# Kernel optimization log

Hardware: AMD Instinct MI355X
Metric: run time of the kernel (lower is better)

Reference implementation:

```python
import jax, jax.numpy as jnp
import numpy as np

# fp4 e2m1 positive value grid and midpoints between adjacent grid values
_GRID = jnp.array([0.0, 0.5, 1.0, 1.5, 2.0, 3.0, 4.0, 6.0], dtype=jnp.float32)
_MIDS = jnp.array([0.25, 0.75, 1.25, 1.75, 2.5, 3.5, 5.0], dtype=jnp.float32)
BLOCK = 32               # MX block size
E8M0_BIAS = 127
F32_MIN_NORMAL = float(2.0 ** -126)
F4_E2M1_MAX_POW2 = 2     # log2 of largest power-of-two <= 6.0 -> 4.0


def _quantize_fp4(a):
    """Round-to-nearest-even onto the signed e2m1 grid."""
    mag = jnp.clip(jnp.abs(a), 0.0, 6.0)
    idx = jnp.searchsorted(_MIDS, mag, side='left')  # ties round down
    mids_pad = jnp.concatenate([_MIDS, jnp.array([-1.0], jnp.float32)])
    tie = mag == mids_pad[idx]
    idx = jnp.where(tie & (idx % 2 == 1), idx + 1, idx)  # ties-to-even mantissa
    return _GRID[idx] * jnp.where(a < 0, -1.0, 1.0)


def _floor_log2(m):
    """Exact floor(log2(m)) for m > 0, with corrections for fp rounding of log2."""
    e = jnp.floor(jnp.log2(m))
    e = jnp.where(jnp.exp2(e) > m, e - 1.0, e)
    e = jnp.where(jnp.exp2(e + 1.0) <= m, e + 1.0, e)
    return e


def _qdq_mxfp4(x):
    """Quantize-dequantize x to MX fp4_e2m1, block 32, FLOOR scale mode (to_mx + to_dtype)."""
    shp = x.shape
    xb = x.reshape(-1, BLOCK)
    max_abs = jnp.max(jnp.abs(xb), axis=1)
    eps = F32_MIN_NORMAL * (max_abs == 0).astype(jnp.float32)
    pow2 = _floor_log2(max_abs + eps)
    e_unb = jnp.clip(pow2 - F4_E2M1_MAX_POW2, -float(E8M0_BIAS), float(E8M0_BIAS) + 1.0)
    scale = jnp.maximum(jnp.exp2(e_unb), F32_MIN_NORMAL)  # [nblk]
    q = _quantize_fp4(xb / scale[:, None])
    return (q * scale[:, None]).reshape(shp)


def _dequant_weight(weight_packed, weight_scale, out_f, in_f):
    """Unpack uint8-packed fp4 (low nibble first), apply e8m0 block scales."""
    p = weight_packed.astype(jnp.int32)
    low = p & 0xF
    high = (p >> 4) & 0xF
    nib = jnp.stack([low, high], axis=-1).reshape(out_f, in_f)  # interleave low,high
    vals = _GRID[nib & 7] * jnp.where((nib & 8) > 0, -1.0, 1.0)
    s = jnp.exp2(weight_scale.astype(jnp.float32) - E8M0_BIAS)  # get_fp_scale(e8m0)
    return (vals.reshape(-1, BLOCK) * s[:, None]).reshape(out_f, in_f)


def setup_inputs() -> dict:
    key = jax.random.key(0)
    k1, k2, k3 = jax.random.split(key, 3)
    M, IN, OUT = 4096, 4096, 4096
    x = jax.random.normal(k1, (M, IN), dtype=jnp.float32)
    weight_packed = jax.random.randint(k2, (OUT, IN // 2), 0, 256, dtype=jnp.int32)
    weight_scale = jax.random.randint(k3, (OUT * IN // BLOCK,), 0, 135, dtype=jnp.int32)
    return {"x": x, "weight_packed": weight_packed, "weight_scale": weight_scale}


def reference(x, weight_packed, weight_scale):
    out_f = weight_packed.shape[0]
    in_f = weight_packed.shape[1] * 2
    xq = _qdq_mxfp4(x)                                       # qdq_mxfp4(x)
    w_dq = _dequant_weight(weight_packed, weight_scale, out_f, in_f)
    return xq @ w_dq.T                                       # matmul(x, w_dq.t())
```

## Files before the change

### kernel.cpp

```cpp
#include <hip/hip_runtime.h>
#include <stdint.h>

typedef __attribute__((ext_vector_type(4)))  int   intx4;
typedef __attribute__((ext_vector_type(8)))  int   intx8;
typedef __attribute__((ext_vector_type(16))) float floatx16;

#define GLL16(gp, lp)                                                               \
    __builtin_amdgcn_global_load_lds((const __attribute__((address_space(1))) unsigned int*)(gp), \
                                     (__attribute__((address_space(3))) unsigned int*)(lp), 16, 0, 0)
#define GLL4(gp, lp)                                                                \
    __builtin_amdgcn_global_load_lds((const __attribute__((address_space(1))) unsigned int*)(gp), \
                                     (__attribute__((address_space(3))) unsigned int*)(lp), 4, 0, 0)

__device__ __forceinline__ uint32_t enc1(float xv, float inv) {
    float a = fminf(fabsf(xv) * inv, 6.0f);
    int e;
    if (a < 2.0f)      e = (int)rintf(a + a);
    else if (a < 4.0f) e = (int)rintf(a) + 2;
    else               e = (int)rintf(a * 0.5f) + 4;
    return (uint32_t)e | ((__float_as_uint(xv) >> 28) & 8u);
}

__global__ __launch_bounds__(256) void quant_x_kernel(const float* __restrict__ x,
                                                      uint32_t* __restrict__ xq,
                                                      uint8_t* __restrict__ xs) {
    const int gl = blockIdx.x * 256 + threadIdx.x;
    const float4 v = ((const float4*)x)[gl];
    float m = fmaxf(fmaxf(fabsf(v.x), fabsf(v.y)), fmaxf(fabsf(v.z), fabsf(v.w)));
    m = fmaxf(m, __shfl_xor(m, 1));
    m = fmaxf(m, __shfl_xor(m, 2));
    m = fmaxf(m, __shfl_xor(m, 4));
    const unsigned ef = __float_as_uint(m) >> 23;
    const unsigned code = (ef < 3u) ? 1u : (ef - 2u);
    const float inv = __uint_as_float((254u - code) << 23);
    const uint32_t p = enc1(v.x, inv)        | (enc1(v.y, inv) << 4)
                     | (enc1(v.z, inv) << 8) | (enc1(v.w, inv) << 12);
    ((uint16_t*)xq)[gl] = (uint16_t)p;
    if ((gl & 7) == 0) xs[gl >> 3] = (uint8_t)code;
}

__global__ __launch_bounds__(256) void repack_kernel(const int* __restrict__ wp,
                                                     uint32_t* __restrict__ wrep,
                                                     int n4w,
                                                     const int* __restrict__ wsc,
                                                     uint32_t* __restrict__ ws,
                                                     int n4s) {
    const int t = blockIdx.x * 256 + threadIdx.x;
    if (t < n4w) {
        const int4 p = ((const int4*)wp)[t];
        wrep[t] = (uint32_t)(p.x & 0xFF) | ((uint32_t)(p.y & 0xFF) << 8)
                | ((uint32_t)(p.z & 0xFF) << 16) | ((uint32_t)(p.w & 0xFF) << 24);
    } else if (t - n4w < n4s) {
        const int i = t - n4w;
        const int4 p = ((const int4*)wsc)[i];
        ws[i] = (uint32_t)(p.x & 0xFF) | ((uint32_t)(p.y & 0xFF) << 8)
              | ((uint32_t)(p.z & 0xFF) << 16) | ((uint32_t)(p.w & 0xFF) << 24);
    }
}

__global__ __launch_bounds__(256) void tpose_s_kernel(const uint8_t* __restrict__ nat,
                                                      uint8_t* __restrict__ xs_t,
                                                      uint8_t* __restrict__ ws_t,
                                                      int R, int Ck) {
    __shared__ uint8_t raw[128 * 32];
    const int r0 = blockIdx.x * 128;
    const int c0 = blockIdx.y * 32;
    const int t = threadIdx.x;
    {
        const int r = t >> 1, hf = t & 1;
        const uint4 v = *(const uint4*)(nat + (size_t)(r0 + r) * Ck + c0 + hf * 16);
        *(uint4*)(raw + r * 32 + hf * 16) = v;
    }
    __syncthreads();
    const int c = t >> 3, q = t & 7;
    uint32_t d[4];
#pragma unroll
    for (int j = 0; j < 4; ++j) {
        const int mb = q * 16 + j * 4;
        d[j] = (uint32_t)raw[(mb + 0) * 32 + c]
             | ((uint32_t)raw[(mb + 1) * 32 + c] << 8)
             | ((uint32_t)raw[(mb + 2) * 32 + c] << 16)
             | ((uint32_t)raw[(mb + 3) * 32 + c] << 24);
    }
    uint8_t* outp = (r0 < R) ? (xs_t + (size_t)(c0 + c) * R + r0)
                             : (ws_t + (size_t)(c0 + c) * R + (r0 - R));
    *(uint4*)(outp + q * 16) = make_uint4(d[0], d[1], d[2], d[3]);
}

__global__ __launch_bounds__(256) void gemm_mx_kernel(const uint8_t* __restrict__ Apk,
                                                      const uint8_t* __restrict__ Bpk,
                                                      const uint8_t* __restrict__ AsT,
                                                      const uint8_t* __restrict__ BsT,
                                                      float* __restrict__ C,
                                                      int M, int N, int K) {
    __shared__ __align__(16) uint8_t sA[16384];
    __shared__ __align__(16) uint8_t sB[16384];
    __shared__ __align__(16) uint8_t sS[2048];

    const int tid = threadIdx.x;
    const int bm0 = blockIdx.y << 7;
    const int bn0 = blockIdx.x << 7;
    const int wave = tid >> 6;
    const int lane = tid & 63;
    const int wm = (wave >> 1) << 6;
    const int wn = (wave & 1) << 6;
    const int row = lane & 31;
    const int h = lane >> 5;
    const int Kb = K >> 1;

    const uint8_t* Ag[4];
    const uint8_t* Bg[4];
#pragma unroll
    for (int i = 0; i < 4; ++i) {
        const int s = tid + 256 * i;
        const int r = s >> 3;
        const int p = (s & 7) ^ (r & 7);
        Ag[i] = Apk + (size_t)(bm0 + r) * Kb + p * 16;
        Bg[i] = Bpk + (size_t)(bn0 + r) * Kb + p * 16;
    }

    const int st = tid & 127;
    const int sj = st >> 5, si = st & 31;
    const size_t sR = (size_t)((tid < 128) ? M : N);
    const uint8_t* Sg1 = ((tid < 128) ? (AsT + (size_t)sj * M + bm0)
                                      : (BsT + (size_t)sj * N + bn0)) + si * 4;
    const uint8_t* Sg2 = Sg1 + 4 * sR;
    const size_t sAdv = 8 * sR;
    const int soff = ((tid < 128) ? 0 : 1024) + st * 4;

    floatx16 acc[2][2];
#pragma unroll
    for (int a = 0; a < 2; ++a)
#pragma unroll
        for (int b = 0; b < 2; ++b)
#pragma unroll
            for (int r = 0; r < 16; ++r) acc[a][b][r] = 0.f;

    const int nchunk = K >> 8;
    const int ar0 = wm + row, ar1 = wm + 32 + row;
    const int br0 = wn + row, br1 = wn + 32 + row;

    for (int c = 0; c < nchunk; ++c) {
        __syncthreads();
        const size_t koff = (size_t)c << 7;
#pragma unroll
        for (int i = 0; i < 4; ++i) GLL16(Ag[i] + koff, sA + (tid + 256 * i) * 16);
#pragma unroll
        for (int i = 0; i < 4; ++i) GLL16(Bg[i] + koff, sB + (tid + 256 * i) * 16);
        GLL4(Sg1 + (size_t)c * sAdv, sS + soff);
        GLL4(Sg2 + (size_t)c * sAdv, sS + soff + 512);
        __syncthreads();

#pragma unroll
        for (int s = 0; s < 4; ++s) {
            const int kp = 2 * s + h;
            intx4 a4[2], b4[2];
            int sa[2], sb[2];
            a4[0] = *(const intx4*)(sA + ar0 * 128 + ((kp ^ (ar0 & 7)) << 4));
            a4[1] = *(const intx4*)(sA + ar1 * 128 + ((kp ^ (ar1 & 7)) << 4));
            b4[0] = *(const intx4*)(sB + br0 * 128 + ((kp ^ (br0 & 7)) << 4));
            b4[1] = *(const intx4*)(sB + br1 * 128 + ((kp ^ (br1 & 7)) << 4));
            sa[0] = sS[kp * 128 + ar0];
            sa[1] = sS[kp * 128 + ar1];
            sb[0] = sS[1024 + kp * 128 + br0];
            sb[1] = sS[1024 + kp * 128 + br1];
#pragma unroll
            for (int mt = 0; mt < 2; ++mt)
#pragma unroll
                for (int nt = 0; nt < 2; ++nt) {
                    intx8 a8 = {a4[mt][0], a4[mt][1], a4[mt][2], a4[mt][3], 0, 0, 0, 0};
                    intx8 b8 = {b4[nt][0], b4[nt][1], b4[nt][2], b4[nt][3], 0, 0, 0, 0};
                    acc[mt][nt] = __builtin_amdgcn_mfma_scale_f32_32x32x64_f8f6f4(
                        a8, b8, acc[mt][nt], 4, 4, 0, sa[mt], 0, sb[nt]);
                }
        }
    }

#pragma unroll
    for (int mt = 0; mt < 2; ++mt)
#pragma unroll
        for (int nt = 0; nt < 2; ++nt) {
            const int col = bn0 + wn + nt * 32 + row;
#pragma unroll
            for (int g = 0; g < 4; ++g) {
                const int rw = bm0 + wm + mt * 32 + 8 * g + 4 * h;
#pragma unroll
                for (int q = 0; q < 4; ++q)
                    C[(size_t)(rw + q) * N + col] = acc[mt][nt][4 * g + q];
            }
        }
}

extern "C" void kernel_launch(void* const* d_in, const int* in_sizes, int n_in,
                              void* d_out, int out_size, void* d_ws, size_t ws_size,
                              hipStream_t stream) {
    const float* x = (const float*)d_in[0];
    const int* wp = (const int*)d_in[1];
    const int* wsc = (const int*)d_in[2];
    float* out = (float*)d_out;

    const int K = 4096;
    const int M = in_sizes[0] / K;
    const int N = (in_sizes[1] * 2) / K;
    const int kbpr = K / 32;
    const int npack = N * K / 2;

    uint32_t* xq   = (uint32_t*)d_ws;
    uint8_t*  xs   = (uint8_t*)d_ws + (size_t)M * K / 2;
    uint8_t*  ws   = xs + (size_t)M * kbpr;
    uint32_t* wrep = (uint32_t*)(ws + (size_t)N * kbpr);
    uint8_t*  xs_t = (uint8_t*)(wrep + (size_t)npack / 4);
    uint8_t*  ws_t = xs_t + (size_t)M * kbpr;

    const int n4w = npack / 4;
    const int n4s = (N * kbpr) / 4;

    quant_x_kernel<<<(M * K / 4) / 256, 256, 0, stream>>>(x, xq, xs);
    repack_kernel<<<(n4w + n4s + 255) / 256, 256, 0, stream>>>(wp, wrep, n4w,
                                                               wsc, (uint32_t*)ws, n4s);
    dim3 tg(2 * M / 128, kbpr / 32);
    tpose_s_kernel<<<tg, 256, 0, stream>>>(xs, xs_t, ws_t, M, kbpr);

    dim3 grid(N / 128, M / 128);
    gemm_mx_kernel<<<grid, 256, 0, stream>>>((const uint8_t*)xq, (const uint8_t*)wrep,
                                             xs_t, ws_t, out, M, N, K);
}
```

Before: 192.3 us.

## Widen GEMM block tile to 128x256 with 64x128 per-wave tiles

Doubles the N extent of each GEMM workgroup to 256 columns, so each wave computes a 64x128 output tile with 8 MFMA accumulators instead of 4. A-tile loads and A-scale loads are reused across twice as many output columns, which cuts global and LDS traffic per MFMA. Global pointers are also replaced by 32-bit offsets to save registers, and launch bounds ask for 3 workgroups per CU. In exchange, LDS use grows to about 52KB per block, accumulator register pressure doubles, and the grid has half as many workgroups.

```diff
diff --git a/kernel.cpp b/kernel.cpp
--- a/kernel.cpp
+++ b/kernel.cpp
@@ -87,87 +87,91 @@
     *(uint4*)(outp + q * 16) = make_uint4(d[0], d[1], d[2], d[3]);
 }
 
-__global__ __launch_bounds__(256) void gemm_mx_kernel(const uint8_t* __restrict__ Apk,
-                                                      const uint8_t* __restrict__ Bpk,
-                                                      const uint8_t* __restrict__ AsT,
-                                                      const uint8_t* __restrict__ BsT,
-                                                      float* __restrict__ C,
-                                                      int M, int N, int K) {
+__global__ __launch_bounds__(256, 3) void gemm_mx_kernel(const uint8_t* __restrict__ Apk,
+                                                         const uint8_t* __restrict__ Bpk,
+                                                         const uint8_t* __restrict__ AsT,
+                                                         const uint8_t* __restrict__ BsT,
+                                                         float* __restrict__ C,
+                                                         int M, int N, int K) {
     __shared__ __align__(16) uint8_t sA[16384];
-    __shared__ __align__(16) uint8_t sB[16384];
-    __shared__ __align__(16) uint8_t sS[2048];
+    __shared__ __align__(16) uint8_t sB[32768];
+    __shared__ __align__(16) uint8_t sS[3072];
 
     const int tid = threadIdx.x;
     const int bm0 = blockIdx.y << 7;
-    const int bn0 = blockIdx.x << 7;
+    const int bn0 = blockIdx.x << 8;
     const int wave = tid >> 6;
     const int lane = tid & 63;
     const int wm = (wave >> 1) << 6;
-    const int wn = (wave & 1) << 6;
+    const int wn = (wave & 1) << 7;
     const int row = lane & 31;
     const int h = lane >> 5;
     const int Kb = K >> 1;
 
-    const uint8_t* Ag[4];
-    const uint8_t* Bg[4];
+    uint32_t aoff[4], boff[8];
 #pragma unroll
     for (int i = 0; i < 4; ++i) {
         const int s = tid + 256 * i;
         const int r = s >> 3;
         const int p = (s & 7) ^ (r & 7);
-        Ag[i] = Apk + (size_t)(bm0 + r) * Kb + p * 16;
-        Bg[i] = Bpk + (size_t)(bn0 + r) * Kb + p * 16;
-    }
-
-    const int st = tid & 127;
-    const int sj = st >> 5, si = st & 31;
-    const size_t sR = (size_t)((tid < 128) ? M : N);
-    const uint8_t* Sg1 = ((tid < 128) ? (AsT + (size_t)sj * M + bm0)
-                                      : (BsT + (size_t)sj * N + bn0)) + si * 4;
-    const uint8_t* Sg2 = Sg1 + 4 * sR;
-    const size_t sAdv = 8 * sR;
-    const int soff = ((tid < 128) ? 0 : 1024) + st * 4;
-
-    floatx16 acc[2][2];
+        aoff[i] = (uint32_t)((bm0 + r) * Kb + p * 16);
+    }
+#pragma unroll
+    for (int i = 0; i < 8; ++i) {
+        const int s = tid + 256 * i;
+        const int r = s >> 3;
+        const int p = (s & 7) ^ (r & 7);
+        boff[i] = (uint32_t)((bn0 + r) * Kb + p * 16);
+    }
+
+    const uint8_t* SgA  = AsT + (size_t)(tid >> 5) * M + bm0 + (tid & 31) * 4;
+    const uint8_t* SgB1 = BsT + (size_t)(tid >> 6) * N + bn0 + (tid & 63) * 4;
+    const uint8_t* SgB2 = SgB1 + (size_t)4 * N;
+    const size_t sAdvA = (size_t)8 * M;
+    const size_t sAdvB = (size_t)8 * N;
+
+    floatx16 acc[2][4];
 #pragma unroll
     for (int a = 0; a < 2; ++a)
 #pragma unroll
-        for (int b = 0; b < 2; ++b)
+        for (int b = 0; b < 4; ++b)
 #pragma unroll
             for (int r = 0; r < 16; ++r) acc[a][b][r] = 0.f;
 
     const int nchunk = K >> 8;
     const int ar0 = wm + row, ar1 = wm + 32 + row;
-    const int br0 = wn + row, br1 = wn + 32 + row;
 
     for (int c = 0; c < nchunk; ++c) {
         __syncthreads();
-        const size_t koff = (size_t)c << 7;
-#pragma unroll
-        for (int i = 0; i < 4; ++i) GLL16(Ag[i] + koff, sA + (tid + 256 * i) * 16);
-#pragma unroll
-        for (int i = 0; i < 4; ++i) GLL16(Bg[i] + koff, sB + (tid + 256 * i) * 16);
-        GLL4(Sg1 + (size_t)c * sAdv, sS + soff);
-        GLL4(Sg2 + (size_t)c * sAdv, sS + soff + 512);
+        const uint32_t koff = (uint32_t)c << 7;
+#pragma unroll
+        for (int i = 0; i < 4; ++i) GLL16(Apk + aoff[i] + koff, sA + (tid + 256 * i) * 16);
+#pragma unroll
+        for (int i = 0; i < 8; ++i) GLL16(Bpk + boff[i] + koff, sB + (tid + 256 * i) * 16);
+        GLL4(SgA  + (size_t)c * sAdvA, sS + tid * 4);
+        GLL4(SgB1 + (size_t)c * sAdvB, sS + 1024 + tid * 4);
+        GLL4(SgB2 + (size_t)c * sAdvB, sS + 2048 + tid * 4);
         __syncthreads();
 
 #pragma unroll
         for (int s = 0; s < 4; ++s) {
             const int kp = 2 * s + h;
-            intx4 a4[2], b4[2];
-            int sa[2], sb[2];
+            intx4 a4[2], b4[4];
+            int sa[2], sb[4];
             a4[0] = *(const intx4*)(sA + ar0 * 128 + ((kp ^ (ar0 & 7)) << 4));
             a4[1] = *(const intx4*)(sA + ar1 * 128 + ((kp ^ (ar1 & 7)) << 4));
-            b4[0] = *(const intx4*)(sB + br0 * 128 + ((kp ^ (br0 & 7)) << 4));
-            b4[1] = *(const intx4*)(sB + br1 * 128 + ((kp ^ (br1 & 7)) << 4));
             sa[0] = sS[kp * 128 + ar0];
             sa[1] = sS[kp * 128 + ar1];
-            sb[0] = sS[1024 + kp * 128 + br0];
-            sb[1] = sS[1024 + kp * 128 + br1];
+#pragma unroll
+            for (int nt = 0; nt < 4; ++nt) {
+                const int br = wn + nt * 32 + row;
+                b4[nt] = *(const intx4*)(sB + br * 128 + ((kp ^ (br & 7)) << 4));
+                sb[nt] = sS[1024 + kp * 256 + br];
+            }
 #pragma unroll
             for (int mt = 0; mt < 2; ++mt)
 #pragma unroll
-                for (int nt = 0; nt < 2; ++nt) {
+                for (int nt = 0; nt < 4; ++nt) {
                     intx8 a8 = {a4[mt][0], a4[mt][1], a4[mt][2], a4[mt][3], 0, 0, 0, 0};
                     intx8 b8 = {b4[nt][0], b4[nt][1], b4[nt][2], b4[nt][3], 0, 0, 0, 0};
                     acc[mt][nt] = __builtin_amdgcn_mfma_scale_f32_32x32x64_f8f6f4(
@@ -179,7 +183,7 @@
 #pragma unroll
     for (int mt = 0; mt < 2; ++mt)
 #pragma unroll
-        for (int nt = 0; nt < 2; ++nt) {
+        for (int nt = 0; nt < 4; ++nt) {
             const int col = bn0 + wn + nt * 32 + row;
 #pragma unroll
             for (int g = 0; g < 4; ++g) {
@@ -221,7 +225,7 @@
     dim3 tg(2 * M / 128, kbpr / 32);
     tpose_s_kernel<<<tg, 256, 0, stream>>>(xs, xs_t, ws_t, M, kbpr);
 
-    dim3 grid(N / 128, M / 128);
+    dim3 grid(N / 256, M / 128);
     gemm_mx_kernel<<<grid, 256, 0, stream>>>((const uint8_t*)xq, (const uint8_t*)wrep,
                                              xs_t, ws_t, out, M, N, K);
 }
```

Measured after the change: 280.3 us. +45.8%, slower.

## Fuse scale transpose into repack kernel and remap GEMM block order across XCDs

Applied to the files above, without the earlier changes.

Merges the weight-scale packing and the scale-transpose kernels into the repack kernel, so weight scales are read straight from the int32 input and transposed in one pass. This drops one launch and the round trip of the intermediate packed-scale buffer. Separately, the GEMM remaps its linear block id so that consecutive tiles are grouped onto the same XCD (stride nwg/8), aiming for better L2 reuse of A/B tiles. The transpose blocks hardcode 64 row-tiles per column group, which only holds for M=N=4096.

```diff
diff --git a/kernel.cpp b/kernel.cpp
--- a/kernel.cpp
+++ b/kernel.cpp
@@ -41,35 +41,39 @@
 
 __global__ __launch_bounds__(256) void repack_kernel(const int* __restrict__ wp,
                                                      uint32_t* __restrict__ wrep,
-                                                     int n4w,
+                                                     int nwb,
+                                                     const uint8_t* __restrict__ xs,
                                                      const int* __restrict__ wsc,
-                                                     uint32_t* __restrict__ ws,
-                                                     int n4s) {
-    const int t = blockIdx.x * 256 + threadIdx.x;
-    if (t < n4w) {
-        const int4 p = ((const int4*)wp)[t];
-        wrep[t] = (uint32_t)(p.x & 0xFF) | ((uint32_t)(p.y & 0xFF) << 8)
+                                                     uint8_t* __restrict__ xs_t,
+                                                     uint8_t* __restrict__ ws_t,
+                                                     int R, int Ck) {
+    const int bid = blockIdx.x;
+    const int t = threadIdx.x;
+    if (bid < nwb) {
+        const int i = bid * 256 + t;
+        const int4 p = ((const int4*)wp)[i];
+        wrep[i] = (uint32_t)(p.x & 0xFF) | ((uint32_t)(p.y & 0xFF) << 8)
                 | ((uint32_t)(p.z & 0xFF) << 16) | ((uint32_t)(p.w & 0xFF) << 24);
-    } else if (t - n4w < n4s) {
-        const int i = t - n4w;
-        const int4 p = ((const int4*)wsc)[i];
-        ws[i] = (uint32_t)(p.x & 0xFF) | ((uint32_t)(p.y & 0xFF) << 8)
-              | ((uint32_t)(p.z & 0xFF) << 16) | ((uint32_t)(p.w & 0xFF) << 24);
-    }
-}
-
-__global__ __launch_bounds__(256) void tpose_s_kernel(const uint8_t* __restrict__ nat,
-                                                      uint8_t* __restrict__ xs_t,
-                                                      uint8_t* __restrict__ ws_t,
-                                                      int R, int Ck) {
+        return;
+    }
     __shared__ uint8_t raw[128 * 32];
-    const int r0 = blockIdx.x * 128;
-    const int c0 = blockIdx.y * 32;
-    const int t = threadIdx.x;
-    {
-        const int r = t >> 1, hf = t & 1;
-        const uint4 v = *(const uint4*)(nat + (size_t)(r0 + r) * Ck + c0 + hf * 16);
+    const int tidx = bid - nwb;
+    const int r0 = (tidx & 63) * 128;
+    const int c0 = (tidx >> 6) * 32;
+    const int r = t >> 1, hf = t & 1;
+    if (r0 < R) {
+        const uint4 v = *(const uint4*)(xs + (size_t)(r0 + r) * Ck + c0 + hf * 16);
         *(uint4*)(raw + r * 32 + hf * 16) = v;
+    } else {
+        const size_t base = (size_t)(r0 - R + r) * Ck + c0 + hf * 16;
+        uint32_t b[4];
+#pragma unroll
+        for (int j = 0; j < 4; ++j) {
+            const int4 p = *(const int4*)(wsc + base + 4 * j);
+            b[j] = (uint32_t)(p.x & 0xFF) | ((uint32_t)(p.y & 0xFF) << 8)
+                 | ((uint32_t)(p.z & 0xFF) << 16) | ((uint32_t)(p.w & 0xFF) << 24);
+        }
+        *(uint4*)(raw + r * 32 + hf * 16) = make_uint4(b[0], b[1], b[2], b[3]);
     }
     __syncthreads();
     const int c = t >> 3, q = t & 7;
@@ -98,8 +102,12 @@
     __shared__ __align__(16) uint8_t sS[2048];
 
     const int tid = threadIdx.x;
-    const int bm0 = blockIdx.y << 7;
-    const int bn0 = blockIdx.x << 7;
+    const int nwg = gridDim.x * gridDim.y;
+    int bid = blockIdx.y * gridDim.x + blockIdx.x;
+    bid = (bid & 7) * (nwg >> 3) + (bid >> 3);
+    const int bn0 = (bid % gridDim.x) << 7;
+    const int bm0 = (bid / gridDim.x) << 7;
+
     const int wave = tid >> 6;
     const int lane = tid & 63;
     const int wm = (wave >> 1) << 6;
@@ -207,19 +215,16 @@
 
     uint32_t* xq   = (uint32_t*)d_ws;
     uint8_t*  xs   = (uint8_t*)d_ws + (size_t)M * K / 2;
-    uint8_t*  ws   = xs + (size_t)M * kbpr;
-    uint32_t* wrep = (uint32_t*)(ws + (size_t)N * kbpr);
+    uint32_t* wrep = (uint32_t*)(xs + (size_t)M * kbpr);
     uint8_t*  xs_t = (uint8_t*)(wrep + (size_t)npack / 4);
     uint8_t*  ws_t = xs_t + (size_t)M * kbpr;
 
-    const int n4w = npack / 4;
-    const int n4s = (N * kbpr) / 4;
+    const int nwb = npack / 4 / 256;
+    const int ntb = (2 * M / 128) * (kbpr / 32);
 
     quant_x_kernel<<<(M * K / 4) / 256, 256, 0, stream>>>(x, xq, xs);
-    repack_kernel<<<(n4w + n4s + 255) / 256, 256, 0, stream>>>(wp, wrep, n4w,
-                                                               wsc, (uint32_t*)ws, n4s);
-    dim3 tg(2 * M / 128, kbpr / 32);
-    tpose_s_kernel<<<tg, 256, 0, stream>>>(xs, xs_t, ws_t, M, kbpr);
+    repack_kernel<<<nwb + ntb, 256, 0, stream>>>(wp, wrep, nwb,
+                                                 xs, wsc, xs_t, ws_t, M, kbpr);
 
     dim3 grid(N / 128, M / 128);
     gemm_mx_kernel<<<grid, 256, 0, stream>>>((const uint8_t*)xq, (const uint8_t*)wrep,
```

Result: slower. 199.6 us (+3.8%).
